# Optimization experiments

Hardware: AMD Instinct MI355X
Metric: run time of the kernel (lower is better)

Reference implementation:

```python
import jax, jax.numpy as jnp
import numpy as np

N = 50000          # total points (25 clouds x 2000 pts)
C = 64             # feature channels (in == out, no bottleneck)
K_NN = 16          # neighbors kept per dilation branch
DILATIONS = (1, 2, 4)
KMAX = K_NN * max(DILATIONS)   # base kNN graph has k*d_max neighbors per node
B = 25             # number of point clouds
EPS = 1e-16


def setup_inputs() -> dict:
    key = jax.random.key(0)
    ks = jax.random.split(key, 8)
    x = jax.random.normal(ks[0], (N, C), jnp.float32)
    pos = jax.random.normal(ks[1], (N, 3), jnp.float32)
    # kNN-style edge_index [2, N*KMAX]: row0 = source/neighbor j, row1 = center i,
    # KMAX consecutive edges per center node, neighbors restricted to the same cloud.
    pts = N // B
    cloud_base = (jnp.arange(N) // pts) * pts
    src = cloud_base[:, None] + jax.random.randint(ks[2], (N, KMAX), 0, pts)
    dst = jnp.broadcast_to(jnp.arange(N)[:, None], (N, KMAX))
    edge_index = jnp.stack([src.reshape(-1), dst.reshape(-1)]).astype(jnp.int32)
    batch = jnp.repeat(jnp.arange(B), pts).astype(jnp.int32)
    nD = len(DILATIONS)
    s = 1.0 / np.sqrt(C)
    Wv = jax.random.normal(ks[3], (nD, C, C), jnp.float32) * s   # lin (value)
    Wq = jax.random.normal(ks[4], (nD, C, C), jnp.float32) * s   # lin_dst
    Wk = jax.random.normal(ks[5], (nD, C, C), jnp.float32) * s   # lin_src
    Wp = jax.random.normal(ks[6], (nD, 3, C), jnp.float32) * (1.0 / np.sqrt(3.0))  # pos_nn
    bp = jax.random.normal(ks[7], (nD, C), jnp.float32) * 0.01
    return dict(x=x, pos=pos, Wv=Wv, Wq=Wq, Wk=Wk, Wp=Wp, bp=bp,
                edge_index=edge_index, batch=batch)


def _dilated_edges(edge_index, k, d):
    # take every d-th of the first k*d neighbors within each node's block -> k edges/node
    e = edge_index.reshape(2, -1, KMAX)[:, :, : k * d : d]
    return e.reshape(2, -1)


def _segment_softmax(a, seg, n):
    amax = jax.ops.segment_max(a, seg, num_segments=n)
    e = jnp.exp(a - amax[seg])
    s = jax.ops.segment_sum(e, seg, num_segments=n)
    return e / (s[seg] + EPS)


def _pt_conv(x, pos, src, dst, Wv, Wq, Wk, Wp, bp):
    # PyG PointTransformerConv: msg = softmax_i(q_i - k_j + delta_ij) * (v_j + delta_ij)
    n = x.shape[0]
    q = x @ Wq        # [N, C]  (lin_dst)
    kk = x @ Wk       # [N, C]  (lin_src)
    v = x @ Wv        # [N, C]  (lin, value)
    delta = (pos[dst] - pos[src]) @ Wp + bp            # [E, C] positional encoding
    alpha = _segment_softmax(q[dst] - kk[src] + delta, dst, n)
    return jax.ops.segment_sum(alpha * (v[src] + delta), dst, num_segments=n)


def reference(x, pos, Wv, Wq, Wk, Wp, bp, edge_index, batch):
    inputs = x
    res = None
    for i, d in enumerate(DILATIONS):
        e = _dilated_edges(edge_index, K_NN, d)
        h = _pt_conv(x, pos, e[0], e[1], Wv[i], Wq[i], Wk[i], Wp[i], bp[i])
        res = h if res is None else jnp.maximum(res, h)   # stack+max over branches
    # global max pool per cloud, gathered back per node
    pool = jax.ops.segment_max(x, batch, num_segments=B)[batch]
    res = jnp.maximum(res, pool)
    return res + inputs   # residual
```

## Files before the change

kernel.cpp:

```cpp
#include <hip/hip_runtime.h>
#include <math.h>

#define NP 50000
#define CH 64
#define KMAX 64
#define KNN 16
#define NB 25
#define PTS (NP / NB)
#define EPSF 1e-16f
#define NTILES (NP / 16)
#define ATILES (NP / 4)
#define TPW 4
#define L2E 1.4426950408889634f
#define LN2 0.6931471805599453f

typedef __attribute__((ext_vector_type(8))) short short8;
typedef __attribute__((ext_vector_type(4))) float float4v;
typedef __attribute__((ext_vector_type(4))) unsigned int uint4v;
typedef __attribute__((ext_vector_type(2))) unsigned int uint2v;
typedef __attribute__((ext_vector_type(4))) unsigned short ushort4v;

__device__ __forceinline__ ushort f2b(float f) {
  unsigned u = __float_as_uint(f);
  unsigned r = (u + 0x7FFFu + ((u >> 16) & 1u)) >> 16;
  return (ushort)r;
}
__device__ __forceinline__ float b2f(ushort h) {
  return __uint_as_float(((unsigned)h) << 16);
}

#define QBF_BYTES   ((size_t)3 * NP * CH * 2)
#define KVP_BYTES   ((size_t)3 * NP * CH * 4)
#define XBF_BYTES   ((size_t)NP * CH * 2)
#define WPACK_ELEMS (9 * 4 * 2 * 64 * 8)
#define XV (NP * CH / 4)

__global__ __launch_bounds__(256) void prep_kernel(
    const float* __restrict__ x,
    const float* __restrict__ Wv,
    const float* __restrict__ Wq,
    const float* __restrict__ Wk,
    ushort* __restrict__ x_bf,
    ushort* __restrict__ wpack,
    float* __restrict__ pool) {
  const int tid = threadIdx.x;
  const int bid = blockIdx.x;
  __shared__ float red[4][CH];

  if (bid < NB) {
    const int lane = tid & 63;
    const int wave = tid >> 6;
    const float* xb = x + (size_t)bid * PTS * CH;
    float m0 = -INFINITY, m1 = -INFINITY, m2 = -INFINITY, m3 = -INFINITY;
    for (int r = wave * 4; r < PTS; r += 16) {
      m0 = fmaxf(m0, xb[(size_t)(r + 0) * CH + lane]);
      m1 = fmaxf(m1, xb[(size_t)(r + 1) * CH + lane]);
      m2 = fmaxf(m2, xb[(size_t)(r + 2) * CH + lane]);
      m3 = fmaxf(m3, xb[(size_t)(r + 3) * CH + lane]);
    }
    red[wave][lane] = fmaxf(fmaxf(m0, m1), fmaxf(m2, m3));
    __syncthreads();
    if (wave == 0) {
      pool[bid * CH + lane] = fmaxf(fmaxf(red[0][lane], red[1][lane]),
                                    fmaxf(red[2][lane], red[3][lane]));
    }
  } else {
    const int gid = (bid - NB) * 256 + tid;
    if (gid < XV) {
      const float4* xv = (const float4*)x;
      float4 v = xv[gid];
      ushort4v o;
      o[0] = f2b(v.x); o[1] = f2b(v.y); o[2] = f2b(v.z); o[3] = f2b(v.w);
      *(ushort4v*)(x_bf + (size_t)gid * 4) = o;
    } else {
      int pid = gid - XV;
      if (pid < WPACK_ELEMS) {
        int j     = pid & 7;
        int lane  = (pid >> 3) & 63;
        int kstep = (pid >> 9) & 1;
        int mtile = (pid >> 10) & 3;
        int mat   = pid >> 12;
        const float* W;
        int d;
        float scale;
        if (mat < 3)      { W = Wq; d = mat;     scale = L2E; }
        else if (mat < 6) { W = Wk; d = mat - 3; scale = L2E; }
        else              { W = Wv; d = mat - 6; scale = 1.f; }
        int oc = mtile * 16 + (lane & 15);
        int ic = kstep * 32 + ((lane >> 4) & 3) * 8 + j;
        wpack[pid] = f2b(W[d * CH * CH + ic * CH + oc] * scale);
      }
    }
  }
}

__global__ __launch_bounds__(256) void qkv_mfma(
    const ushort* __restrict__ x_bf,
    const ushort* __restrict__ wpack,
    ushort* __restrict__ qbf,
    unsigned int* __restrict__ kvp) {
  const int lane = threadIdx.x;
  const int wave = threadIdx.y;
  const int dd   = blockIdx.y;
  const int kbase = (lane >> 4) * 8;
  const int tile0 = (blockIdx.x * 4 + wave) * TPW;

  short8 afQ[4][2], afK[4][2], afV[4][2];
#pragma unroll
  for (int mt = 0; mt < 4; ++mt)
#pragma unroll
    for (int ks = 0; ks < 2; ++ks) {
      afQ[mt][ks] = *(const short8*)(wpack +
          ((((size_t)dd * 4 + mt) * 2 + ks) * 64 + lane) * 8);
      afK[mt][ks] = *(const short8*)(wpack +
          ((((size_t)(3 + dd) * 4 + mt) * 2 + ks) * 64 + lane) * 8);
      afV[mt][ks] = *(const short8*)(wpack +
          ((((size_t)(6 + dd) * 4 + mt) * 2 + ks) * 64 + lane) * 8);
    }

  ushort* outQ = qbf + (size_t)dd * NP * CH;
  unsigned int* outKV = kvp + (size_t)dd * NP * CH;

#pragma unroll
  for (int t = 0; t < TPW; ++t) {
    int tile = tile0 + t;
    if (tile >= NTILES) break;
    int myNode = tile * 16 + (lane & 15);
    const ushort* xr = x_bf + (size_t)myNode * CH;
    short8 b0 = *(const short8*)(xr + kbase);
    short8 b1 = *(const short8*)(xr + 32 + kbase);
#pragma unroll
    for (int mt = 0; mt < 4; ++mt) {
      float4v aQ = {0.f, 0.f, 0.f, 0.f};
      aQ = __builtin_amdgcn_mfma_f32_16x16x32_bf16(afQ[mt][0], b0, aQ, 0, 0, 0);
      aQ = __builtin_amdgcn_mfma_f32_16x16x32_bf16(afQ[mt][1], b1, aQ, 0, 0, 0);
      int oc = mt * 16 + (lane >> 4) * 4;
      uint2v oq;
      oq[0] = (unsigned)f2b(aQ[0]) | ((unsigned)f2b(aQ[1]) << 16);
      oq[1] = (unsigned)f2b(aQ[2]) | ((unsigned)f2b(aQ[3]) << 16);
      *(uint2v*)(outQ + (size_t)myNode * CH + oc) = oq;
    }
#pragma unroll
    for (int mt = 0; mt < 4; ++mt) {
      float4v aK = {0.f, 0.f, 0.f, 0.f};
      float4v aV = {0.f, 0.f, 0.f, 0.f};
      aK = __builtin_amdgcn_mfma_f32_16x16x32_bf16(afK[mt][0], b0, aK, 0, 0, 0);
      aK = __builtin_amdgcn_mfma_f32_16x16x32_bf16(afK[mt][1], b1, aK, 0, 0, 0);
      aV = __builtin_amdgcn_mfma_f32_16x16x32_bf16(afV[mt][0], b0, aV, 0, 0, 0);
      aV = __builtin_amdgcn_mfma_f32_16x16x32_bf16(afV[mt][1], b1, aV, 0, 0, 0);
      int oc = mt * 16 + (lane >> 4) * 4;
      uint4v o;
#pragma unroll
      for (int i = 0; i < 4; ++i)
        o[i] = ((unsigned)f2b(aK[i]) << 16) | (unsigned)f2b(aV[i]);
      *(uint4v*)(outKV + (size_t)myNode * CH + oc) = o;
    }
  }
}

__global__ __launch_bounds__(192) void attn_kernel(
    const float* __restrict__ x,
    const float* __restrict__ pos,
    const float* __restrict__ Wp,
    const float* __restrict__ bp,
    const int*   __restrict__ edge_src,
    const ushort* __restrict__ qbf,
    const unsigned int* __restrict__ kvp,
    const float* __restrict__ pool,
    float* __restrict__ out) {
  const int bx  = blockIdx.x;
  const int xcd = bx & 7;
  const int kk  = bx >> 3;
  const int base = (ATILES * xcd) >> 3;
  const int cnt  = ((ATILES * (xcd + 1)) >> 3) - base;
  if (kk >= cnt) return;
  const int node0 = (base + kk) * 4;

  const int tid = threadIdx.y * 64 + threadIdx.x;
  __shared__ float sEdge[4 * 260];
  __shared__ float sRes[2 * 4 * 68];

  for (int r = tid; r < 4 * KMAX; r += 192) {
    int nl = r >> 6, p = r & 63;
    int nd = node0 + nl;
    int j = edge_src[(size_t)nd * KMAX + p];
    float4v w;
    w[0] = pos[nd * 3 + 0] - pos[j * 3 + 0];
    w[1] = pos[nd * 3 + 1] - pos[j * 3 + 1];
    w[2] = pos[nd * 3 + 2] - pos[j * 3 + 2];
    w[3] = __int_as_float(j << 8);
    *(float4v*)&sEdge[nl * 260 + p * 4] = w;
  }
  __syncthreads();

  const int dd   = threadIdx.y;
  const int lane = threadIdx.x;
  const int g    = lane >> 4;
  const int cl   = lane & 15;
  const int node = node0 + g;
  const float* sMy = &sEdge[g * 260];
  const unsigned clOfs = (unsigned)(cl << 4);

  float4v q, bq, wp0, wp1, wp2;
  {
    ushort4v qh = *(const ushort4v*)(qbf + ((size_t)dd * NP + node) * CH + cl * 4);
#pragma unroll
    for (int i = 0; i < 4; ++i) q[i] = b2f(qh[i]);
    const float* WpD = Wp + dd * 192;
    wp0 = *(const float4v*)(WpD + 0 * 64 + cl * 4) * L2E;
    wp1 = *(const float4v*)(WpD + 1 * 64 + cl * 4) * L2E;
    wp2 = *(const float4v*)(WpD + 2 * 64 + cl * 4) * L2E;
    float4v bpv = *(const float4v*)(bp + dd * 64 + cl * 4);
    bq = q + bpv * L2E;
  }
  const char* KVb = (const char*)(kvp + (size_t)dd * NP * CH);

  float4v s    = {0.f, 0.f, 0.f, 0.f};
  float4v accv = {0.f, 0.f, 0.f, 0.f};
  float4v acct = {0.f, 0.f, 0.f, 0.f};
#pragma unroll
  for (int e = 0; e < KNN; ++e) {
    const int p = e << dd;
    float4v w = *(const float4v*)(sMy + p * 4);
    uint4v u = *(const uint4v*)(KVb + (__float_as_uint(w[3]) + clOfs));
    float4v kf, vf, wgt;
#pragma unroll
    for (int i = 0; i < 4; ++i) kf[i] = __uint_as_float(u[i] & 0xFFFF0000u);
#pragma unroll
    for (int i = 0; i < 4; ++i) vf[i] = __uint_as_float(u[i] << 16);
    float4v t = bq + w[0] * wp0 + w[1] * wp1 + w[2] * wp2;
    float4v a = t - kf;
#pragma unroll
    for (int i = 0; i < 4; ++i) wgt[i] = __builtin_amdgcn_exp2f(a[i]);
    s    += wgt;
    accv += wgt * vf;
    acct += wgt * t;
  }
  float4v r;
#pragma unroll
  for (int i = 0; i < 4; ++i) {
    float accd = acct[i] - q[i] * s[i];
    r[i] = (accv[i] + LN2 * accd) * __builtin_amdgcn_rcpf(s[i] + EPSF);
  }

  if (dd > 0)
    *(float4v*)&sRes[((dd - 1) * 4 + g) * 68 + cl * 4] = r;
  __syncthreads();
  if (dd == 0) {
    float4v r1 = *(const float4v*)&sRes[(0 * 4 + g) * 68 + cl * 4];
    float4v r2 = *(const float4v*)&sRes[(1 * 4 + g) * 68 + cl * 4];
    const int b = node / PTS;
    float4v pv = *(const float4v*)(pool + b * CH + cl * 4);
    float4v xv = *(const float4v*)(x + (size_t)node * CH + cl * 4);
    float4v res;
#pragma unroll
    for (int i = 0; i < 4; ++i)
      res[i] = fmaxf(fmaxf(fmaxf(r[i], r1[i]), r2[i]), pv[i]) + xv[i];
    *(float4v*)(out + (size_t)node * CH + cl * 4) = res;
  }
}

extern "C" void kernel_launch(void* const* d_in, const int* in_sizes, int n_in,
                              void* d_out, int out_size, void* d_ws, size_t ws_size,
                              hipStream_t stream) {
  const float* x    = (const float*)d_in[0];
  const float* pos  = (const float*)d_in[1];
  const float* Wv   = (const float*)d_in[2];
  const float* Wq   = (const float*)d_in[3];
  const float* Wk   = (const float*)d_in[4];
  const float* Wp   = (const float*)d_in[5];
  const float* bp   = (const float*)d_in[6];
  const int*   ei   = (const int*)d_in[7];
  float* out = (float*)d_out;

  char* wsb = (char*)d_ws;
  ushort* qbf   = (ushort*)wsb;
  unsigned int* kvp = (unsigned int*)(wsb + QBF_BYTES);
  ushort* x_bf  = (ushort*)(wsb + QBF_BYTES + KVP_BYTES);
  ushort* wpack = (ushort*)(wsb + QBF_BYTES + KVP_BYTES + XBF_BYTES);
  float*  pool  = (float*)(wsb + QBF_BYTES + KVP_BYTES + XBF_BYTES +
                           (size_t)WPACK_ELEMS * 2);

  {
    int convBlocks = (XV + WPACK_ELEMS + 255) / 256;
    dim3 grid(NB + convBlocks);
    hipLaunchKernelGGL(prep_kernel, grid, dim3(256), 0, stream,
                       x, Wv, Wq, Wk, x_bf, wpack, pool);
  }
  {
    dim3 grid((NTILES + 4 * TPW - 1) / (4 * TPW), 3);
    dim3 block(64, 4);
    hipLaunchKernelGGL(qkv_mfma, grid, block, 0, stream, x_bf, wpack, qbf, kvp);
  }
  {
    dim3 grid(8 * ((ATILES + 7) / 8));
    dim3 block(64, 3);
    hipLaunchKernelGGL(attn_kernel, grid, block, 0, stream,
                       x, pos, Wp, bp, ei, qbf, kvp, pool, out);
  }
}
```

Before: 226.3 us.

## Split attention edges across two waves and spread QKV projection over more blocks

```diff
diff --git a/kernel.cpp b/kernel.cpp
--- a/kernel.cpp
+++ b/kernel.cpp
@@ -10,7 +10,6 @@
 #define EPSF 1e-16f
 #define NTILES (NP / 16)
 #define ATILES (NP / 4)
-#define TPW 4
 #define L2E 1.4426950408889634f
 #define LN2 0.6931471805599453f
 
@@ -100,54 +99,52 @@
     ushort* __restrict__ qbf,
     unsigned int* __restrict__ kvp) {
   const int lane = threadIdx.x;
-  const int wave = threadIdx.y;
-  const int dd   = blockIdx.y;
+  const int tile = blockIdx.x * 4 + threadIdx.y;
+  if (tile >= NTILES) return;
+  const int y = blockIdx.y;
   const int kbase = (lane >> 4) * 8;
-  const int tile0 = (blockIdx.x * 4 + wave) * TPW;
-
-  short8 afQ[4][2], afK[4][2], afV[4][2];
-#pragma unroll
-  for (int mt = 0; mt < 4; ++mt)
-#pragma unroll
-    for (int ks = 0; ks < 2; ++ks) {
-      afQ[mt][ks] = *(const short8*)(wpack +
-          ((((size_t)dd * 4 + mt) * 2 + ks) * 64 + lane) * 8);
-      afK[mt][ks] = *(const short8*)(wpack +
-          ((((size_t)(3 + dd) * 4 + mt) * 2 + ks) * 64 + lane) * 8);
-      afV[mt][ks] = *(const short8*)(wpack +
-          ((((size_t)(6 + dd) * 4 + mt) * 2 + ks) * 64 + lane) * 8);
-    }
-
-  ushort* outQ = qbf + (size_t)dd * NP * CH;
-  unsigned int* outKV = kvp + (size_t)dd * NP * CH;
-
-#pragma unroll
-  for (int t = 0; t < TPW; ++t) {
-    int tile = tile0 + t;
-    if (tile >= NTILES) break;
-    int myNode = tile * 16 + (lane & 15);
-    const ushort* xr = x_bf + (size_t)myNode * CH;
-    short8 b0 = *(const short8*)(xr + kbase);
-    short8 b1 = *(const short8*)(xr + 32 + kbase);
+  const int myNode = tile * 16 + (lane & 15);
+  const ushort* xr = x_bf + (size_t)myNode * CH;
+  short8 b0 = *(const short8*)(xr + kbase);
+  short8 b1 = *(const short8*)(xr + 32 + kbase);
+
+  if (y < 3) {
+    const int dd = y;
+    ushort* outQ = qbf + (size_t)dd * NP * CH;
 #pragma unroll
     for (int mt = 0; mt < 4; ++mt) {
-      float4v aQ = {0.f, 0.f, 0.f, 0.f};
-      aQ = __builtin_amdgcn_mfma_f32_16x16x32_bf16(afQ[mt][0], b0, aQ, 0, 0, 0);
-      aQ = __builtin_amdgcn_mfma_f32_16x16x32_bf16(afQ[mt][1], b1, aQ, 0, 0, 0);
+      short8 a0 = *(const short8*)(wpack +
+          ((((size_t)dd * 4 + mt) * 2 + 0) * 64 + lane) * 8);
+      short8 a1 = *(const short8*)(wpack +
+          ((((size_t)dd * 4 + mt) * 2 + 1) * 64 + lane) * 8);
+      float4v acc = {0.f, 0.f, 0.f, 0.f};
+      acc = __builtin_amdgcn_mfma_f32_16x16x32_bf16(a0, b0, acc, 0, 0, 0);
+      acc = __builtin_amdgcn_mfma_f32_16x16x32_bf16(a1, b1, acc, 0, 0, 0);
       int oc = mt * 16 + (lane >> 4) * 4;
-      uint2v oq;
-      oq[0] = (unsigned)f2b(aQ[0]) | ((unsigned)f2b(aQ[1]) << 16);
-      oq[1] = (unsigned)f2b(aQ[2]) | ((unsigned)f2b(aQ[3]) << 16);
-      *(uint2v*)(outQ + (size_t)myNode * CH + oc) = oq;
-    }
+      uint2v o;
+      o[0] = (unsigned)f2b(acc[0]) | ((unsigned)f2b(acc[1]) << 16);
+      o[1] = (unsigned)f2b(acc[2]) | ((unsigned)f2b(acc[3]) << 16);
+      *(uint2v*)(outQ + (size_t)myNode * CH + oc) = o;
+    }
+  } else {
+    const int dd = y - 3;
+    unsigned int* outKV = kvp + (size_t)dd * NP * CH;
 #pragma unroll
     for (int mt = 0; mt < 4; ++mt) {
+      short8 k0 = *(const short8*)(wpack +
+          ((((size_t)(3 + dd) * 4 + mt) * 2 + 0) * 64 + lane) * 8);
+      short8 k1 = *(const short8*)(wpack +
+          ((((size_t)(3 + dd) * 4 + mt) * 2 + 1) * 64 + lane) * 8);
+      short8 v0 = *(const short8*)(wpack +
+          ((((size_t)(6 + dd) * 4 + mt) * 2 + 0) * 64 + lane) * 8);
+      short8 v1 = *(const short8*)(wpack +
+          ((((size_t)(6 + dd) * 4 + mt) * 2 + 1) * 64 + lane) * 8);
       float4v aK = {0.f, 0.f, 0.f, 0.f};
       float4v aV = {0.f, 0.f, 0.f, 0.f};
-      aK = __builtin_amdgcn_mfma_f32_16x16x32_bf16(afK[mt][0], b0, aK, 0, 0, 0);
-      aK = __builtin_amdgcn_mfma_f32_16x16x32_bf16(afK[mt][1], b1, aK, 0, 0, 0);
-      aV = __builtin_amdgcn_mfma_f32_16x16x32_bf16(afV[mt][0], b0, aV, 0, 0, 0);
-      aV = __builtin_amdgcn_mfma_f32_16x16x32_bf16(afV[mt][1], b1, aV, 0, 0, 0);
+      aK = __builtin_amdgcn_mfma_f32_16x16x32_bf16(k0, b0, aK, 0, 0, 0);
+      aK = __builtin_amdgcn_mfma_f32_16x16x32_bf16(k1, b1, aK, 0, 0, 0);
+      aV = __builtin_amdgcn_mfma_f32_16x16x32_bf16(v0, b0, aV, 0, 0, 0);
+      aV = __builtin_amdgcn_mfma_f32_16x16x32_bf16(v1, b1, aV, 0, 0, 0);
       int oc = mt * 16 + (lane >> 4) * 4;
       uint4v o;
 #pragma unroll
@@ -158,7 +155,7 @@
   }
 }
 
-__global__ __launch_bounds__(192) void attn_kernel(
+__global__ __launch_bounds__(384, 6) void attn_kernel(
     const float* __restrict__ x,
     const float* __restrict__ pos,
     const float* __restrict__ Wp,
@@ -176,12 +173,18 @@
   if (kk >= cnt) return;
   const int node0 = (base + kk) * 4;
 
-  const int tid = threadIdx.y * 64 + threadIdx.x;
+  const int wy   = threadIdx.y;
+  const int dd   = wy % 3;
+  const int half = wy / 3;
+  const int tid  = wy * 64 + threadIdx.x;
+
   __shared__ float sEdge[4 * 260];
+  __shared__ float sPartS[3 * 4 * 68];
+  __shared__ float sPartA[3 * 4 * 68];
   __shared__ float sRes[2 * 4 * 68];
 
-  for (int r = tid; r < 4 * KMAX; r += 192) {
-    int nl = r >> 6, p = r & 63;
+  if (tid < 256) {
+    int nl = tid >> 6, p = tid & 63;
     int nd = node0 + nl;
     int j = edge_src[(size_t)nd * KMAX + p];
     float4v w;
@@ -193,7 +196,6 @@
   }
   __syncthreads();
 
-  const int dd   = threadIdx.y;
   const int lane = threadIdx.x;
   const int g    = lane >> 4;
   const int cl   = lane & 15;
@@ -201,26 +203,24 @@
   const float* sMy = &sEdge[g * 260];
   const unsigned clOfs = (unsigned)(cl << 4);
 
-  float4v q, bq, wp0, wp1, wp2;
+  float4v bq, wp0, wp1, wp2;
   {
     ushort4v qh = *(const ushort4v*)(qbf + ((size_t)dd * NP + node) * CH + cl * 4);
-#pragma unroll
-    for (int i = 0; i < 4; ++i) q[i] = b2f(qh[i]);
     const float* WpD = Wp + dd * 192;
     wp0 = *(const float4v*)(WpD + 0 * 64 + cl * 4) * L2E;
     wp1 = *(const float4v*)(WpD + 1 * 64 + cl * 4) * L2E;
     wp2 = *(const float4v*)(WpD + 2 * 64 + cl * 4) * L2E;
     float4v bpv = *(const float4v*)(bp + dd * 64 + cl * 4);
-    bq = q + bpv * L2E;
+#pragma unroll
+    for (int i = 0; i < 4; ++i) bq[i] = b2f(qh[i]) + bpv[i] * L2E;
   }
   const char* KVb = (const char*)(kvp + (size_t)dd * NP * CH);
 
   float4v s    = {0.f, 0.f, 0.f, 0.f};
   float4v accv = {0.f, 0.f, 0.f, 0.f};
-  float4v acct = {0.f, 0.f, 0.f, 0.f};
-#pragma unroll
-  for (int e = 0; e < KNN; ++e) {
-    const int p = e << dd;
+#pragma unroll
+  for (int e = 0; e < 8; ++e) {
+    const int p = (half * 8 + e) << dd;
     float4v w = *(const float4v*)(sMy + p * 4);
     uint4v u = *(const uint4v*)(KVb + (__float_as_uint(w[3]) + clOfs));
     float4v kf, vf, wgt;
@@ -232,21 +232,37 @@
     float4v a = t - kf;
 #pragma unroll
     for (int i = 0; i < 4; ++i) wgt[i] = __builtin_amdgcn_exp2f(a[i]);
-    s    += wgt;
-    accv += wgt * vf;
-    acct += wgt * t;
-  }
+    s += wgt;
+    float4v vt;
+#pragma unroll
+    for (int i = 0; i < 4; ++i) vt[i] = fmaf(LN2, t[i], vf[i]);
+    accv += wgt * vt;
+  }
+
+  if (half == 1) {
+    *(float4v*)&sPartS[(dd * 4 + g) * 68 + cl * 4] = s;
+    *(float4v*)&sPartA[(dd * 4 + g) * 68 + cl * 4] = accv;
+  }
+  __syncthreads();
+
   float4v r;
-#pragma unroll
-  for (int i = 0; i < 4; ++i) {
-    float accd = acct[i] - q[i] * s[i];
-    r[i] = (accv[i] + LN2 * accd) * __builtin_amdgcn_rcpf(s[i] + EPSF);
-  }
-
-  if (dd > 0)
-    *(float4v*)&sRes[((dd - 1) * 4 + g) * 68 + cl * 4] = r;
+  if (half == 0) {
+    float4v s2 = *(const float4v*)&sPartS[(dd * 4 + g) * 68 + cl * 4];
+    float4v a2 = *(const float4v*)&sPartA[(dd * 4 + g) * 68 + cl * 4];
+    s += s2;
+    accv += a2;
+    float4v bpv = *(const float4v*)(bp + dd * 64 + cl * 4);
+#pragma unroll
+    for (int i = 0; i < 4; ++i) {
+      float q = (bq[i] - bpv[i] * L2E) * LN2;
+      r[i] = accv[i] * __builtin_amdgcn_rcpf(s[i] + EPSF) - q;
+    }
+    if (dd > 0)
+      *(float4v*)&sRes[((dd - 1) * 4 + g) * 68 + cl * 4] = r;
+  }
   __syncthreads();
-  if (dd == 0) {
+
+  if (wy == 0) {
     float4v r1 = *(const float4v*)&sRes[(0 * 4 + g) * 68 + cl * 4];
     float4v r2 = *(const float4v*)&sRes[(1 * 4 + g) * 68 + cl * 4];
     const int b = node / PTS;
@@ -288,13 +304,13 @@
                        x, Wv, Wq, Wk, x_bf, wpack, pool);
   }
   {
-    dim3 grid((NTILES + 4 * TPW - 1) / (4 * TPW), 3);
+    dim3 grid((NTILES + 3) / 4, 6);
     dim3 block(64, 4);
     hipLaunchKernelGGL(qkv_mfma, grid, block, 0, stream, x_bf, wpack, qbf, kvp);
   }
   {
     dim3 grid(8 * ((ATILES + 7) / 8));
-    dim3 block(64, 3);
+    dim3 block(64, 6);
     hipLaunchKernelGGL(attn_kernel, grid, block, 0, stream,
                        x, pos, Wp, bp, ei, qbf, kvp, pool, out);
   }
```

After: 218.2 us. 3.6% less time.
